# Performance work log

Hardware: AMD Instinct MI355X
Metric: run time of the kernel (lower is better)

## Reference

```python
import jax, jax.numpy as jnp
import numpy as np

N_NODES = 100_000
N_EDGES = 1_600_000
IN_CH = 128
HIDDEN = 48
OUT_CH = 16
NEG_SLOPE = 0.2  # PyG GATConv default LeakyReLU slope


def setup_inputs() -> dict:
    key = jax.random.key(0)
    ks = jax.random.split(key, 8)
    x = jax.random.normal(ks[0], (N_NODES, IN_CH), dtype=jnp.float32)
    edge_index = jax.random.randint(ks[1], (2, N_EDGES), 0, N_NODES, dtype=jnp.int64)
    W = jax.random.normal(ks[2], (IN_CH, HIDDEN), dtype=jnp.float32) / np.sqrt(IN_CH)
    att_src = jax.random.normal(ks[3], (HIDDEN,), dtype=jnp.float32) / np.sqrt(HIDDEN)
    att_dst = jax.random.normal(ks[4], (HIDDEN,), dtype=jnp.float32) / np.sqrt(HIDDEN)
    gat_bias = jax.random.normal(ks[5], (HIDDEN,), dtype=jnp.float32) * 0.01
    lin_W = jax.random.normal(ks[6], (HIDDEN, OUT_CH), dtype=jnp.float32) / np.sqrt(HIDDEN)
    lin_b = jax.random.normal(ks[7], (OUT_CH,), dtype=jnp.float32) * 0.01
    return {"x": x, "edge_index": edge_index, "W": W, "att_src": att_src,
            "att_dst": att_dst, "gat_bias": gat_bias, "lin_W": lin_W, "lin_b": lin_b}


def reference(x, edge_index, W, att_src, att_dst, gat_bias, lin_W, lin_b):
    n = x.shape[0]
    # PyG GATConv adds self loops by default
    loops = jnp.arange(n, dtype=edge_index.dtype)
    src = jnp.concatenate([edge_index[0], loops])  # [E+N] message sources j
    dst = jnp.concatenate([edge_index[1], loops])  # [E+N] message targets i

    h = x @ W                      # [N, H] transformed node features
    a_src = h @ att_src            # [N] per-node source attention term
    a_dst = h @ att_dst            # [N] per-node destination attention term

    logits = jax.nn.leaky_relu(a_src[src] + a_dst[dst], NEG_SLOPE)  # [E+N]
    # segment softmax over incoming edges of each destination node
    m = jax.ops.segment_max(logits, dst, num_segments=n)            # [N]
    e = jnp.exp(logits - m[dst])
    denom = jax.ops.segment_sum(e, dst, num_segments=n)             # [N] (>0: self loop)
    alpha = e / denom[dst]                                          # [E+N]

    agg = jax.ops.segment_sum(h[src] * alpha[:, None], dst, num_segments=n)
    out = jax.nn.elu(agg + gat_bias)          # [N, H]
    # dropout is identity in eval mode
    z = out @ lin_W + lin_b                   # [N, OUT]
    return jax.nn.log_softmax(z, axis=-1)
```

## Files before the change

kernel.cpp:

```cpp
#include <hip/hip_runtime.h>
#include <hip/hip_fp16.h>

#define IN_CH 128
#define HID 48
#define OUT_CH 16
#define NEG_SLOPE 0.2f
#define SCAN_ELEMS 2048
#define ROWB 128
#define WLP 20

__device__ __forceinline__ float leaky(float x) { return x >= 0.f ? x : NEG_SLOPE * x; }
__device__ __forceinline__ float elu(float x) { return x > 0.f ? x : __expf(x) - 1.f; }

__device__ __forceinline__ void load_edge(const void* ei, int E, int is64, int e,
                                          int& s, int& d) {
    if (is64) {
        const long long* p = (const long long*)ei;
        s = (int)p[e];
        d = (int)p[(size_t)E + e];
    } else {
        const int* p = (const int*)ei;
        s = p[e];
        d = p[(size_t)E + e];
    }
}

__global__ __launch_bounds__(256) void k_init(const unsigned* __restrict__ ei,
                                              int* __restrict__ deg,
                                              int* __restrict__ flag, int N) {
    int i = blockIdx.x * blockDim.x + threadIdx.x;
    if (i < N) deg[i] = 0;
    if (i == 0) {
        unsigned sdet = 0;
        for (int k = 1; k < 128; k += 2) sdet |= ei[k];
        *flag = (sdet == 0) ? 1 : 0;
    }
}

#define BLK_NODES 256
__global__ __launch_bounds__(256, 2) void k_xw(const float* __restrict__ x,
                                               const float* __restrict__ W,
                                               const float* __restrict__ att_src,
                                               const float* __restrict__ att_dst,
                                               const void* __restrict__ ei,
                                               __half* __restrict__ h2,
                                               float* __restrict__ a_src,
                                               float* __restrict__ a_dst,
                                               int* __restrict__ deg,
                                               const int* __restrict__ flag,
                                               unsigned short* __restrict__ rank,
                                               int N, int E) {
    __shared__ float Wl[IN_CH * HID];
    __shared__ float xl[BLK_NODES * 33];
    const int t = threadIdx.x;
    for (int i = t; i < IN_CH * HID / 4; i += 256)
        ((float4*)Wl)[i] = ((const float4*)W)[i];
    const int n0 = blockIdx.x * BLK_NODES;
    const int kq = t & 3;
    const int ng = t >> 2;
    const int k0 = kq * 12;

    float acc[4][12];
#pragma unroll
    for (int i = 0; i < 4; ++i)
#pragma unroll
        for (int j = 0; j < 12; ++j) acc[i][j] = 0.f;

    for (int c0 = 0; c0 < IN_CH; c0 += 32) {
        __syncthreads();
#pragma unroll
        for (int p = 0; p < 8; ++p) {
            int id = t + p * 256;
            int row = id >> 3;
            int seg = id & 7;
            int n = n0 + row;
            float4 v = make_float4(0.f, 0.f, 0.f, 0.f);
            if (n < N) v = ((const float4*)(x + (size_t)n * IN_CH + c0))[seg];
            float* dst = &xl[row * 33 + seg * 4];
            dst[0] = v.x; dst[1] = v.y; dst[2] = v.z; dst[3] = v.w;
        }
        __syncthreads();
#pragma unroll 8
        for (int cc = 0; cc < 32; ++cc) {
            int c = c0 + cc;
            float xv[4];
#pragma unroll
            for (int i = 0; i < 4; ++i) xv[i] = xl[(ng * 4 + i) * 33 + cc];
            const float* wr = &Wl[c * HID + k0];
#pragma unroll
            for (int j = 0; j < 12; ++j) {
                float wv = wr[j];
#pragma unroll
                for (int i = 0; i < 4; ++i) acc[i][j] += xv[i] * wv;
            }
        }
    }
#pragma unroll
    for (int i = 0; i < 4; ++i) {
        int n = n0 + ng * 4 + i;
        if (n < N) {
            uint* dst = (uint*)((char*)h2 + (size_t)n * ROWB) + k0 / 2;
#pragma unroll
            for (int j = 0; j < 6; ++j) {
                __half2 hv = __floats2half2_rn(acc[i][2 * j], acc[i][2 * j + 1]);
                dst[j] = *(const uint*)&hv;
            }
        }
    }
#pragma unroll
    for (int p = 0; p < 8; ++p) {
        int id = t + p * 256;
        int row = id >> 3;
        int seg = id & 7;
        int n = n0 + row;
        if (n < N) ((uint*)((char*)h2 + (size_t)n * ROWB))[24 + seg] = 0u;
    }
    float as_[4], ad_[4];
#pragma unroll
    for (int i = 0; i < 4; ++i) {
        float s1 = 0.f, s2 = 0.f;
#pragma unroll
        for (int j = 0; j < 12; ++j) {
            float a = acc[i][j];
            s1 += a * att_src[k0 + j];
            s2 += a * att_dst[k0 + j];
        }
        s1 += __shfl_xor(s1, 1); s1 += __shfl_xor(s1, 2);
        s2 += __shfl_xor(s2, 1); s2 += __shfl_xor(s2, 2);
        as_[i] = s1; ad_[i] = s2;
    }
    if (kq == 0) {
#pragma unroll
        for (int i = 0; i < 4; ++i) {
            int n = n0 + ng * 4 + i;
            if (n < N) { a_src[n] = as_[i]; a_dst[n] = ad_[i]; }
        }
    }
    {
        const int nb = gridDim.x;
        const int per = (E + nb - 1) / nb;
        const int e0 = blockIdx.x * per;
        const int e1 = (e0 + per < E) ? e0 + per : E;
        const int is64 = *flag;
        for (int e = e0 + t; e < e1; e += 256) {
            int d = is64 ? (int)((const long long*)ei)[(size_t)E + e]
                         : ((const int*)ei)[(size_t)E + e];
            rank[e] = (unsigned short)atomicAdd(&deg[d], 1);
        }
    }
}

__global__ __launch_bounds__(256) void k_scan_block(const int* __restrict__ deg,
                                                    int* __restrict__ rowptr,
                                                    int* __restrict__ bsum, int N) {
    __shared__ int sm[256];
    const int t = threadIdx.x;
    const int base = blockIdx.x * SCAN_ELEMS + t * 8;
    int v[8];
    int s = 0;
#pragma unroll
    for (int i = 0; i < 8; ++i) {
        v[i] = (base + i < N) ? deg[base + i] : 0;
        s += v[i];
    }
    sm[t] = s;
    __syncthreads();
    for (int off = 1; off < 256; off <<= 1) {
        int y = (t >= off) ? sm[t - off] : 0;
        __syncthreads();
        sm[t] += y;
        __syncthreads();
    }
    int run = sm[t] - s;
#pragma unroll
    for (int i = 0; i < 8; ++i) {
        if (base + i < N) rowptr[base + i] = run;
        run += v[i];
    }
    if (t == 255) bsum[blockIdx.x] = sm[255];
}

__global__ __launch_bounds__(256) void k_scan_add(int* __restrict__ rowptr,
                                                  const int* __restrict__ bsum, int N, int E) {
    __shared__ int soff;
    const int chunk = (int)(((long long)blockIdx.x * 256) / SCAN_ELEMS);
    if (threadIdx.x == 0) {
        int run = 0;
        for (int b = 0; b < chunk; ++b) run += bsum[b];
        soff = run;
    }
    __syncthreads();
    int i = blockIdx.x * 256 + threadIdx.x;
    if (i == 0) rowptr[N] = E;
    if (i >= N) return;
    rowptr[i] += soff;
}

__global__ __launch_bounds__(256) void k_scatter(const void* __restrict__ ei,
                                                 const int* __restrict__ flag,
                                                 const int* __restrict__ rowptr,
                                                 const unsigned short* __restrict__ rank,
                                                 unsigned* __restrict__ srcs, int E) {
    int e = blockIdx.x * blockDim.x + threadIdx.x;
    if (e >= E) return;
    int is64 = *flag;
    int s, d;
    load_edge(ei, E, is64, e, s, d);
    int pos = rowptr[d] + (int)rank[e];
    srcs[pos] = (unsigned)s;
}

__global__ __launch_bounds__(256) void k_gat_node(const int* __restrict__ rowptr,
                                                  const unsigned* __restrict__ srcs,
                                                  const float* __restrict__ a_src,
                                                  const float* __restrict__ a_dst,
                                                  const __half* __restrict__ h2,
                                                  const float* __restrict__ gat_bias,
                                                  const float* __restrict__ lin_W,
                                                  const float* __restrict__ lin_b,
                                                  float* __restrict__ out, int N) {
    __shared__ float Wl[HID * WLP];
    __shared__ float lb[OUT_CH];
    __shared__ float gb[HID];
    __shared__ float o_sm[4][HID];
    __shared__ unsigned long long evb[4][64];
    const int t = threadIdx.x;
    for (int i = t; i < HID * OUT_CH; i += 256) Wl[(i >> 4) * WLP + (i & 15)] = lin_W[i];
    if (t < OUT_CH) lb[t] = lin_b[t];
    if (t >= 64 && t < 64 + HID) gb[t - 64] = gat_bias[t - 64];
    __syncthreads();

    const int wv = t >> 6;
    const int lane = t & 63;
    const int slot = lane >> 4;
    const int c = lane & 15;
    const int n = blockIdx.x * 4 + wv;
    const bool active = n < N;

    if (active) {
        const int base = rowptr[n];
        const int deg = rowptr[n + 1] - base;
        const float adn = a_dst[n];
        const float ev_self = __expf(fminf(leaky(a_src[n] + adn), 50.f));
        const char* hb = (const char*)h2;

        float a0 = 0.f, a1 = 0.f, a2 = 0.f, a3 = 0.f;
        float evsum = (lane == 0) ? ev_self : 0.f;
        if (slot == 0) {
            uint2 hv = *(const uint2*)(hb + (size_t)n * ROWB + 8 * c);
            __half2 h01 = *(const __half2*)&hv.x;
            __half2 h23 = *(const __half2*)&hv.y;
            a0 = ev_self * __low2float(h01);
            a1 = ev_self * __high2float(h01);
            a2 = ev_self * __low2float(h23);
            a3 = ev_self * __high2float(h23);
        }
        for (int c0 = 0; c0 < deg; c0 += 64) {
            int j = c0 + lane;
            unsigned s = 0;
            float ev = 0.f;
            if (j < deg) {
                s = srcs[base + j];
                ev = __expf(fminf(leaky(a_src[s] + adn), 50.f));
            }
            evsum += ev;
            evb[wv][lane] = ((unsigned long long)__float_as_uint(ev) << 32) | s;
            const int cnt = (deg - c0 < 64) ? (deg - c0) : 64;
            int jj = slot;
            unsigned long long prA = 0;
            uint2 hvA = make_uint2(0u, 0u);
            if (jj < cnt) {
                prA = evb[wv][jj];
                hvA = *(const uint2*)(hb + (size_t)(unsigned)prA * ROWB + 8 * c);
            }
#pragma unroll 2
            for (; jj + 4 < cnt; jj += 4) {
                unsigned long long prB = evb[wv][jj + 4];
                uint2 hvB = *(const uint2*)(hb + (size_t)(unsigned)prB * ROWB + 8 * c);
                float evj = __uint_as_float((unsigned)(prA >> 32));
                __half2 h01 = *(const __half2*)&hvA.x;
                __half2 h23 = *(const __half2*)&hvA.y;
                a0 += evj * __low2float(h01);
                a1 += evj * __high2float(h01);
                a2 += evj * __low2float(h23);
                a3 += evj * __high2float(h23);
                prA = prB; hvA = hvB;
            }
            if (jj < cnt) {
                float evj = __uint_as_float((unsigned)(prA >> 32));
                __half2 h01 = *(const __half2*)&hvA.x;
                __half2 h23 = *(const __half2*)&hvA.y;
                a0 += evj * __low2float(h01);
                a1 += evj * __high2float(h01);
                a2 += evj * __low2float(h23);
                a3 += evj * __high2float(h23);
            }
        }
#pragma unroll
        for (int off = 1; off < 64; off <<= 1) evsum += __shfl_xor(evsum, off);
        a0 += __shfl_xor(a0, 16); a0 += __shfl_xor(a0, 32);
        a1 += __shfl_xor(a1, 16); a1 += __shfl_xor(a1, 32);
        a2 += __shfl_xor(a2, 16); a2 += __shfl_xor(a2, 32);
        a3 += __shfl_xor(a3, 16); a3 += __shfl_xor(a3, 32);
        const float inv = 1.f / evsum;
        if (slot == 0 && c < 12) {
            float4 v = make_float4(elu(a0 * inv + gb[4 * c + 0]),
                                   elu(a1 * inv + gb[4 * c + 1]),
                                   elu(a2 * inv + gb[4 * c + 2]),
                                   elu(a3 * inv + gb[4 * c + 3]));
            *(float4*)&o_sm[wv][4 * c] = v;
        }
    }
    __syncthreads();

    if (active) {
        const float* o = o_sm[wv];
        float z = 0.f;
#pragma unroll
        for (int i = 0; i < 12; ++i) {
            int k = 12 * slot + i;
            z += o[k] * Wl[k * WLP + c];
        }
        z += __shfl_xor(z, 16); z += __shfl_xor(z, 32);
        z += lb[c];
        float mx = z;
#pragma unroll
        for (int off = 8; off; off >>= 1) mx = fmaxf(mx, __shfl_xor(mx, off, 16));
        float ev = __expf(z - mx);
#pragma unroll
        for (int off = 8; off; off >>= 1) ev += __shfl_xor(ev, off, 16);
        float lse = mx + __logf(ev);
        if (slot == 0) out[(size_t)n * OUT_CH + c] = z - lse;
    }
}

extern "C" void kernel_launch(void* const* d_in, const int* in_sizes, int n_in,
                              void* d_out, int out_size, void* d_ws, size_t ws_size,
                              hipStream_t stream) {
    const float* x = (const float*)d_in[0];
    const void* edge_index = d_in[1];
    const float* W = (const float*)d_in[2];
    const float* att_src = (const float*)d_in[3];
    const float* att_dst = (const float*)d_in[4];
    const float* gat_bias = (const float*)d_in[5];
    const float* lin_W = (const float*)d_in[6];
    const float* lin_b = (const float*)d_in[7];
    float* out = (float*)d_out;

    const int N = in_sizes[0] / IN_CH;
    const int E = in_sizes[1] / 2;

    __half* h2 = (__half*)d_ws;
    float* a_src = (float*)((char*)d_ws + (size_t)N * ROWB);
    float* a_dst = a_src + N;
    int* rowptr = (int*)(a_dst + N);
    int* degbuf = rowptr + N + 1;
    int* bsum = degbuf + N;
    int* flag = bsum + 64;
    unsigned short* rank = (unsigned short*)(flag + 1);
    unsigned* srcs =
        (unsigned*)(((uintptr_t)(rank + E) + 3) & ~(uintptr_t)3);

    const int nodeBlocks = (N + 255) / 256;
    const int edgeBlocks = (E + 255) / 256;
    const int scanBlocks = (N + SCAN_ELEMS - 1) / SCAN_ELEMS;

    k_init<<<nodeBlocks, 256, 0, stream>>>((const unsigned*)edge_index, degbuf, flag, N);
    k_xw<<<(N + BLK_NODES - 1) / BLK_NODES, 256, 0, stream>>>(
        x, W, att_src, att_dst, edge_index, h2, a_src, a_dst, degbuf, flag, rank, N, E);
    k_scan_block<<<scanBlocks, 256, 0, stream>>>(degbuf, rowptr, bsum, N);
    k_scan_add<<<nodeBlocks, 256, 0, stream>>>(rowptr, bsum, N, E);
    k_scatter<<<edgeBlocks, 256, 0, stream>>>(edge_index, flag, rowptr, rank, srcs, E);
    k_gat_node<<<(N + 3) / 4, 256, 0, stream>>>(rowptr, srcs, a_src, a_dst,
                                                h2, gat_bias, lin_W, lin_b, out, N);
}
```

Before: 206.9 us.

## Split degree counting out of the GEMM kernel and fold init into it

Removes the separate init kernel by moving degree zeroing and the index-width flag detection into the feature-transform kernel. The per-edge degree atomics, which previously ran in a tail loop of the GEMM kernel's ~391 blocks, now run in their own fully parallel kernel with one thread per edge. This aims to spread the atomic counting across many more threads instead of serialising it behind the GEMM. In exchange it adds a separate launch and requires every block of the GEMM kernel to finish zeroing before counting starts.

```diff
diff --git a/kernel.cpp b/kernel.cpp
--- a/kernel.cpp
+++ b/kernel.cpp
@@ -25,34 +25,25 @@
     }
 }
 
-__global__ __launch_bounds__(256) void k_init(const unsigned* __restrict__ ei,
-                                              int* __restrict__ deg,
-                                              int* __restrict__ flag, int N) {
-    int i = blockIdx.x * blockDim.x + threadIdx.x;
-    if (i < N) deg[i] = 0;
-    if (i == 0) {
-        unsigned sdet = 0;
-        for (int k = 1; k < 128; k += 2) sdet |= ei[k];
-        *flag = (sdet == 0) ? 1 : 0;
-    }
-}
-
 #define BLK_NODES 256
 __global__ __launch_bounds__(256, 2) void k_xw(const float* __restrict__ x,
                                                const float* __restrict__ W,
                                                const float* __restrict__ att_src,
                                                const float* __restrict__ att_dst,
-                                               const void* __restrict__ ei,
+                                               const unsigned* __restrict__ ei,
                                                __half* __restrict__ h2,
                                                float* __restrict__ a_src,
                                                float* __restrict__ a_dst,
                                                int* __restrict__ deg,
-                                               const int* __restrict__ flag,
-                                               unsigned short* __restrict__ rank,
-                                               int N, int E) {
+                                               int* __restrict__ flag, int N) {
     __shared__ float Wl[IN_CH * HID];
     __shared__ float xl[BLK_NODES * 33];
     const int t = threadIdx.x;
+    if (blockIdx.x == 0 && t == 0) {
+        unsigned sdet = 0;
+        for (int i = 1; i < 128; i += 2) sdet |= ei[i];
+        *flag = (sdet == 0) ? 1 : 0;
+    }
     for (int i = t; i < IN_CH * HID / 4; i += 256)
         ((float4*)Wl)[i] = ((const float4*)W)[i];
     const int n0 = blockIdx.x * BLK_NODES;
@@ -137,17 +128,20 @@
         }
     }
     {
-        const int nb = gridDim.x;
-        const int per = (E + nb - 1) / nb;
-        const int e0 = blockIdx.x * per;
-        const int e1 = (e0 + per < E) ? e0 + per : E;
-        const int is64 = *flag;
-        for (int e = e0 + t; e < e1; e += 256) {
-            int d = is64 ? (int)((const long long*)ei)[(size_t)E + e]
-                         : ((const int*)ei)[(size_t)E + e];
-            rank[e] = (unsigned short)atomicAdd(&deg[d], 1);
-        }
-    }
+        int n = n0 + t;
+        if (n < N) deg[n] = 0;
+    }
+}
+
+__global__ __launch_bounds__(256) void k_count(const void* __restrict__ ei,
+                                               const int* __restrict__ flag,
+                                               int* __restrict__ deg,
+                                               unsigned short* __restrict__ rank, int E) {
+    int e = blockIdx.x * blockDim.x + threadIdx.x;
+    if (e >= E) return;
+    int d = (*flag) ? (int)((const long long*)ei)[(size_t)E + e]
+                    : ((const int*)ei)[(size_t)E + e];
+    rank[e] = (unsigned short)atomicAdd(&deg[d], 1);
 }
 
 __global__ __launch_bounds__(256) void k_scan_block(const int* __restrict__ deg,
@@ -365,9 +359,10 @@
     const int edgeBlocks = (E + 255) / 256;
     const int scanBlocks = (N + SCAN_ELEMS - 1) / SCAN_ELEMS;
 
-    k_init<<<nodeBlocks, 256, 0, stream>>>((const unsigned*)edge_index, degbuf, flag, N);
     k_xw<<<(N + BLK_NODES - 1) / BLK_NODES, 256, 0, stream>>>(
-        x, W, att_src, att_dst, edge_index, h2, a_src, a_dst, degbuf, flag, rank, N, E);
+        x, W, att_src, att_dst, (const unsigned*)edge_index,
+        h2, a_src, a_dst, degbuf, flag, N);
+    k_count<<<edgeBlocks, 256, 0, stream>>>(edge_index, flag, degbuf, rank, E);
     k_scan_block<<<scanBlocks, 256, 0, stream>>>(degbuf, rowptr, bsum, N);
     k_scan_add<<<nodeBlocks, 256, 0, stream>>>(rowptr, bsum, N, E);
     k_scatter<<<edgeBlocks, 256, 0, stream>>>(edge_index, flag, rowptr, rank, srcs, E);
```

Result: no change. 208.2 us, median of 2 (+0.6%).
